# Kernel optimization log

Measured on AMD Instinct MI355X. Metric: run time of the kernel, lower is better.

## Reference

```python
import jax, jax.numpy as jnp
import numpy as np

D_MODEL = 512
N_STATE = 64
EMB_DIM = 512
LN_EPS = 1e-5


def setup_inputs() -> dict:
    key = jax.random.key(0)
    ks = jax.random.split(key, 12)
    B, L, d, N, e = 8, 2048, D_MODEL, N_STATE, EMB_DIM
    x = jax.random.normal(ks[0], (B, L, d), dtype=jnp.float32)
    emb = jax.random.normal(ks[1], (B, e), dtype=jnp.float32)
    # S4D kernel params
    A_real = -0.5 * jnp.ones((d, N), dtype=jnp.float32)
    A_imag = jnp.pi * jnp.broadcast_to(jnp.arange(N, dtype=jnp.float32)[None, :], (d, N))
    C = jax.random.normal(ks[2], (d, N, 2), dtype=jnp.float32) * 0.5
    dt_min, dt_max = 0.001, 0.1
    log_dt = jax.random.uniform(ks[3], (d,), dtype=jnp.float32) * (np.log(dt_max) - np.log(dt_min)) + np.log(dt_min)
    B_ssm = jnp.ones((d, N), dtype=jnp.float32)  # buffer, treated as constant
    # block params
    D_skip = jax.random.normal(ks[4], (d,), dtype=jnp.float32) * 0.01
    ln_gamma = jnp.ones((d,), dtype=jnp.float32)
    ln_beta = jnp.zeros((d,), dtype=jnp.float32)
    lim_out = 1.0 / np.sqrt(d)
    W_out = jax.random.uniform(ks[5], (2 * d, d), dtype=jnp.float32, minval=-lim_out, maxval=lim_out)
    b_out = jax.random.uniform(ks[6], (2 * d,), dtype=jnp.float32, minval=-lim_out, maxval=lim_out)
    lim_f = 1.0 / np.sqrt(e)
    W_film = jax.random.uniform(ks[7], (2 * d, e), dtype=jnp.float32, minval=-lim_f, maxval=lim_f)
    b_film = jax.random.uniform(ks[8], (2 * d,), dtype=jnp.float32, minval=-lim_f, maxval=lim_f)
    return dict(x=x, emb=emb, A_real=A_real, A_imag=A_imag, C=C, log_dt=log_dt,
                B_ssm=B_ssm, D_skip=D_skip, ln_gamma=ln_gamma, ln_beta=ln_beta,
                W_out=W_out, b_out=b_out, W_film=W_film, b_film=b_film)


def reference(x, emb, A_real, A_imag, C, log_dt, B_ssm, D_skip, ln_gamma, ln_beta,
              W_out, b_out, W_film, b_film):
    Bsz, L, d = x.shape
    residual = x
    # LayerNorm
    mu = jnp.mean(x, axis=-1, keepdims=True)
    var = jnp.mean((x - mu) ** 2, axis=-1, keepdims=True)
    xn = (x - mu) * jax.lax.rsqrt(var + LN_EPS) * ln_gamma + ln_beta
    # S4D kernel: K[d,l] = Re( sum_n (C*B)[d,n] * exp(dt*A)[d,n]**l ) * dt[d]
    dt = jnp.exp(log_dt)                                 # (d,)
    A = A_real + 1j * A_imag                             # (d,N)
    dtA = A * dt[:, None]                                # (d,N)
    Cc = (C[..., 0] + 1j * C[..., 1]) * B_ssm            # (d,N) complex
    l = jnp.arange(L, dtype=jnp.float32)
    powers = jnp.exp(dtA[:, :, None] * l)                # (d,N,L) complex, A_bar**l
    K = jnp.einsum('dn,dnl->dl', Cc, powers).real * dt[:, None]  # (d,L)
    # FFT convolution (circular over 2L -> linear)
    x_t = jnp.transpose(xn, (0, 2, 1))                   # (B,d,L)
    K_f = jnp.fft.rfft(K, n=2 * L)                       # (d,L+1)
    x_f = jnp.fft.rfft(x_t, n=2 * L)                     # (B,d,L+1)
    y = jnp.fft.irfft(K_f[None] * x_f, n=2 * L)[..., :L] # (B,d,L)
    y = y + x_t * D_skip[None, :, None]
    y = jnp.transpose(y, (0, 2, 1))                      # (B,L,d)
    # FiLM conditioning
    film = jax.nn.silu(emb) @ W_film.T + b_film          # (B,2d)
    scale, shift = jnp.split(film, 2, axis=-1)
    y = y * (1.0 + scale[:, None, :]) + shift[:, None, :]
    # out_proj: Linear(d,2d) + GLU
    proj = y @ W_out.T + b_out                           # (B,L,2d)
    a, g = jnp.split(proj, 2, axis=-1)
    y = a * jax.nn.sigmoid(g)
    return residual + y
```

## Files before the change

### kernel.cpp

```cpp
#include <hip/hip_runtime.h>
#include <math.h>

typedef __attribute__((ext_vector_type(8))) short bf8v;
typedef __attribute__((ext_vector_type(4))) float f4v;

union BF8 { bf8v v; unsigned short e[8]; };

__device__ __forceinline__ float bf2f(unsigned short u) {
  union { unsigned int i; float f; } c; c.i = ((unsigned int)u) << 16; return c.f;
}
__device__ __forceinline__ unsigned short f2bf(float f) {
  union { float f; unsigned int i; } c; c.f = f;
  return (unsigned short)((c.i + 0x7fffu + ((c.i >> 16) & 1u)) >> 16);
}
__device__ __forceinline__ void gld16(const unsigned short* g, unsigned short* l) {
  __builtin_amdgcn_global_load_lds(
      (const __attribute__((address_space(1))) unsigned int*)g,
      (__attribute__((address_space(3))) unsigned int*)l, 16, 0, 0);
}

__global__ __launch_bounds__(256) void prelude_kernel(
    const float* __restrict__ emb, const float* __restrict__ Wf,
    const float* __restrict__ bfm, float* __restrict__ film,
    const float* __restrict__ W, unsigned short* __restrict__ Wb,
    const float* __restrict__ A_real, const float* __restrict__ A_imag,
    const float* __restrict__ Cc, const float* __restrict__ log_dt,
    const float* __restrict__ B_ssm, const float* __restrict__ D_skip,
    unsigned short* __restrict__ Pre, unsigned short* __restrict__ Pim,
    unsigned short* __restrict__ Mre, unsigned short* __restrict__ Mim,
    unsigned short* __restrict__ Tt, float* __restrict__ W64r, float* __restrict__ W64i) {
  __shared__ float Ktl[64];
  const int blk = blockIdx.x;
  const int tid = threadIdx.x;
  if (blk < 2048) {
    const int gw = blk * 4 + (tid >> 6);
    const int lane = tid & 63;
    const int b = gw >> 10, j = gw & 1023;
    const float4* ep = (const float4*)(emb + (size_t)b * 512) + lane * 2;
    const float4* wp = (const float4*)(Wf + (size_t)j * 512) + lane * 2;
    float acc = 0.f;
    #pragma unroll
    for (int i = 0; i < 2; i++) {
      const float4 e = ep[i], w = wp[i];
      acc += (e.x / (1.f + __expf(-e.x))) * w.x;
      acc += (e.y / (1.f + __expf(-e.y))) * w.y;
      acc += (e.z / (1.f + __expf(-e.z))) * w.z;
      acc += (e.w / (1.f + __expf(-e.w))) * w.w;
    }
    #pragma unroll
    for (int off = 32; off >= 1; off >>= 1) acc += __shfl_xor(acc, off);
    if (lane == 0) film[(size_t)b * 1024 + j] = acc + bfm[j];
  } else if (blk < 2560) {
    const int i = (blk - 2048) * 256 + tid;
    const float4 v = ((const float4*)W)[i];
    uint2 pk;
    pk.x = (unsigned)f2bf(v.x) | ((unsigned)f2bf(v.y) << 16);
    pk.y = (unsigned)f2bf(v.z) | ((unsigned)f2bf(v.w) << 16);
    ((uint2*)Wb)[i] = pk;
  } else {
    const int d = blk - 2560;
    const float dt = __expf(log_dt[d]);
    const int wv = tid >> 6, n = tid & 63;
    {
      const int dn = d * 64 + n;
      const float ar = dt * A_real[dn], ai = dt * A_imag[dn];
      const float bs = B_ssm[dn] * dt;
      const float c0 = Cc[dn * 2] * bs, c1 = Cc[dn * 2 + 1] * bs;
      #pragma unroll
      for (int i = 0; i < 16; i++) {
        const float tau = (float)(wv * 16 + i);
        const float ex = __expf(ar * tau);
        float sn, cs; __sincosf(ai * tau, &sn, &cs);
        float r = ex * (c0 * cs - c1 * sn);
        #pragma unroll
        for (int off = 32; off >= 1; off >>= 1) r += __shfl_xor(r, off);
        if (n == 0) Ktl[wv * 16 + i] = (wv * 16 + i == 0) ? (r + D_skip[d]) : r;
      }
    }
    __syncthreads();
    for (int g = tid; g < 512; g += 256) {
      const int nn = g >> 3, s0 = (g & 7) * 8;
      const int dn = d * 64 + nn;
      const float ar = dt * A_real[dn], ai = dt * A_imag[dn];
      union { unsigned short s[8]; uint4 u; } pr, pi;
      #pragma unroll
      for (int j = 0; j < 8; j++) {
        const float k = (float)(63 - (s0 + j));
        const float ex = __expf(ar * k);
        float sn, cs; __sincosf(ai * k, &sn, &cs);
        pr.s[j] = f2bf(ex * cs); pi.s[j] = f2bf(ex * sn);
      }
      *(uint4*)(Pre + (size_t)d * 4096 + nn * 64 + s0) = pr.u;
      *(uint4*)(Pim + (size_t)d * 4096 + nn * 64 + s0) = pi.u;
    }
    for (int g = tid; g < 512; g += 256) {
      const int t = g >> 3, n0 = (g & 7) * 8;
      union { unsigned short s[8]; uint4 u; } mr, mi;
      #pragma unroll
      for (int j = 0; j < 8; j++) {
        const int dn = d * 64 + n0 + j;
        const float ar = dt * A_real[dn], ai = dt * A_imag[dn];
        const float bs = B_ssm[dn] * dt;
        const float c0 = Cc[dn * 2] * bs, c1 = Cc[dn * 2 + 1] * bs;
        const float k = (float)(t + 1);
        const float ex = __expf(ar * k);
        float sn, cs; __sincosf(ai * k, &sn, &cs);
        mr.s[j] = f2bf(ex * (c0 * cs - c1 * sn));
        mi.s[j] = f2bf(-ex * (c0 * sn + c1 * cs));
      }
      *(uint4*)(Mre + (size_t)d * 4096 + t * 64 + n0) = mr.u;
      *(uint4*)(Mim + (size_t)d * 4096 + t * 64 + n0) = mi.u;
    }
    for (int g = tid; g < 512; g += 256) {
      const int t = g >> 3, s0 = (g & 7) * 8;
      union { unsigned short s[8]; uint4 u; } tv;
      #pragma unroll
      for (int j = 0; j < 8; j++) {
        const int s = s0 + j;
        tv.s[j] = (s <= t) ? f2bf(Ktl[t - s]) : (unsigned short)0;
      }
      *(uint4*)(Tt + (size_t)d * 4096 + t * 64 + s0) = tv.u;
    }
    if (tid < 64) {
      const int dn = d * 64 + tid;
      const float ex = __expf(dt * A_real[dn] * 64.f);
      float sn, cs; __sincosf(dt * A_imag[dn] * 64.f, &sn, &cs);
      W64r[d * 64 + tid] = ex * cs;
      W64i[d * 64 + tid] = ex * sn;
    }
  }
}

__global__ __launch_bounds__(256) void lnt_kernel(const float* __restrict__ x,
    const float* __restrict__ gamma, const float* __restrict__ beta,
    unsigned short* __restrict__ xT) {
  __shared__ __align__(16) unsigned short t[16 * 520];
  const int r0 = blockIdx.x * 16;
  const int tid = threadIdx.x, wv = tid >> 6, lane = tid & 63;
  const float4* gp = (const float4*)gamma + lane * 2;
  const float4* bp = (const float4*)beta  + lane * 2;
  const float4 g0 = gp[0], g1 = gp[1], bb0 = bp[0], bb1 = bp[1];
  #pragma unroll
  for (int i = 0; i < 4; i++) {
    const int r = wv * 4 + i;
    const float4* xr = (const float4*)(x + (size_t)(r0 + r) * 512) + lane * 2;
    const float4 v0 = xr[0], v1 = xr[1];
    float s  = v0.x + v0.y + v0.z + v0.w + v1.x + v1.y + v1.z + v1.w;
    float sq = v0.x*v0.x + v0.y*v0.y + v0.z*v0.z + v0.w*v0.w
             + v1.x*v1.x + v1.y*v1.y + v1.z*v1.z + v1.w*v1.w;
    #pragma unroll
    for (int off = 32; off >= 1; off >>= 1) {
      s  += __shfl_xor(s, off);
      sq += __shfl_xor(sq, off);
    }
    const float mu   = s * (1.f / 512.f);
    const float var  = sq * (1.f / 512.f) - mu * mu;
    const float rstd = rsqrtf(var + 1e-5f);
    uint4 pk;
    pk.x = (unsigned)f2bf((v0.x - mu) * rstd * g0.x + bb0.x)
         | ((unsigned)f2bf((v0.y - mu) * rstd * g0.y + bb0.y) << 16);
    pk.y = (unsigned)f2bf((v0.z - mu) * rstd * g0.z + bb0.z)
         | ((unsigned)f2bf((v0.w - mu) * rstd * g0.w + bb0.w) << 16);
    pk.z = (unsigned)f2bf((v1.x - mu) * rstd * g1.x + bb1.x)
         | ((unsigned)f2bf((v1.y - mu) * rstd * g1.y + bb1.y) << 16);
    pk.w = (unsigned)f2bf((v1.z - mu) * rstd * g1.z + bb1.z)
         | ((unsigned)f2bf((v1.w - mu) * rstd * g1.w + bb1.w) << 16);
    *(uint4*)&t[r * 520 + lane * 8] = pk;
  }
  __syncthreads();
  const int p = tid;
  union { unsigned short s[8]; uint4 u; } a0, a1, b0, b1;
  #pragma unroll
  for (int r = 0; r < 8; r++) {
    const unsigned v = *(const unsigned*)&t[r * 520 + p * 2];
    a0.s[r] = (unsigned short)(v & 0xffffu);
    b0.s[r] = (unsigned short)(v >> 16);
  }
  #pragma unroll
  for (int r = 0; r < 8; r++) {
    const unsigned v = *(const unsigned*)&t[(r + 8) * 520 + p * 2];
    a1.s[r] = (unsigned short)(v & 0xffffu);
    b1.s[r] = (unsigned short)(v >> 16);
  }
  unsigned short* o0 = xT + (size_t)(2 * p) * 16384 + r0;
  *(uint4*)o0 = a0.u; *(uint4*)(o0 + 8) = a1.u;
  unsigned short* o1 = xT + (size_t)(2 * p + 1) * 16384 + r0;
  *(uint4*)o1 = b0.u; *(uint4*)(o1 + 8) = b1.u;
}

__global__ __launch_bounds__(256) void tr_kernel(const unsigned short* __restrict__ in,
    unsigned short* __restrict__ out, int R, int C) {
  __shared__ __align__(16) unsigned short t[64 * 72];
  const int c0 = blockIdx.x * 64, r0 = blockIdx.y * 64;
  const int tid = threadIdx.x;
  #pragma unroll
  for (int i = 0; i < 2; i++) {
    const int idx = tid + i * 256;
    const int r = idx >> 3, q = idx & 7;
    const uint4 v = *(const uint4*)(in + (size_t)(r0 + r) * C + c0 + q * 8);
    *(uint4*)&t[r * 72 + ((q ^ (r >> 3)) * 8)] = v;
  }
  __syncthreads();
  #pragma unroll
  for (int i = 0; i < 2; i++) {
    const int idx = tid + i * 256;
    const int c = idx >> 3, g = idx & 7;
    union { unsigned short s[8]; uint4 u; } pk;
    #pragma unroll
    for (int j = 0; j < 8; j++)
      pk.s[j] = t[(g * 8 + j) * 72 + (((c >> 3) ^ g) * 8) + (c & 7)];
    *(uint4*)(out + (size_t)(c0 + c) * R + r0 + g * 8) = pk.u;
  }
}

__global__ __launch_bounds__(256, 4) void ssm_kernel(
    const unsigned short* __restrict__ xT,
    const unsigned short* __restrict__ Pre, const unsigned short* __restrict__ Pim,
    const unsigned short* __restrict__ Mre, const unsigned short* __restrict__ Mim,
    const unsigned short* __restrict__ Tt,
    const float* __restrict__ W64r, const float* __restrict__ W64i,
    const float* __restrict__ film, unsigned short* __restrict__ y2) {
  __shared__ unsigned int Eb[64 * 66];
  __shared__ unsigned short Ibr[64 * 72], Ibi[64 * 72];

  const int bx = blockIdx.x;
  const int d = bx & 511, h = bx >> 9;
  const int tid = threadIdx.x;
  const int wv = tid >> 6, lane = tid & 63;
  const int n15 = lane & 15, quad = lane >> 4;
  const int j0 = wv * 16;
  const int jg0 = h * 64;
  const size_t dtab = (size_t)d * 4096;

  bf8v Xf[2];
  #pragma unroll
  for (int kq = 0; kq < 2; kq++)
    Xf[kq] = *(const bf8v*)(xT + (size_t)d * 16384 + (jg0 + j0 + n15) * 64 + kq * 32 + quad * 8);

  {
    f4v Er[4], Ei[4];
    #pragma unroll
    for (int a = 0; a < 4; a++) { Er[a] = (f4v){0,0,0,0}; Ei[a] = (f4v){0,0,0,0}; }
    #pragma unroll
    for (int mt = 0; mt < 4; mt++)
      #pragma unroll
      for (int kq = 0; kq < 2; kq++) {
        const bf8v pr = *(const bf8v*)(Pre + dtab + (mt * 16 + n15) * 64 + kq * 32 + quad * 8);
        const bf8v pi = *(const bf8v*)(Pim + dtab + (mt * 16 + n15) * 64 + kq * 32 + quad * 8);
        Er[mt] = __builtin_amdgcn_mfma_f32_16x16x32_bf16(pr, Xf[kq], Er[mt], 0, 0, 0);
        Ei[mt] = __builtin_amdgcn_mfma_f32_16x16x32_bf16(pi, Xf[kq], Ei[mt], 0, 0, 0);
      }
    #pragma unroll
    for (int mt = 0; mt < 4; mt++)
      #pragma unroll
      for (int i = 0; i < 4; i++) {
        const int row = mt * 16 + quad * 4 + i;
        Eb[row * 66 + j0 + n15] =
            (unsigned)f2bf(Er[mt][i]) | ((unsigned)f2bf(Ei[mt][i]) << 16);
      }
  }
  __syncthreads();

  {
    const int n = tid & 63, bp = tid >> 6;
    if (bp < 2) {
      const float wre = W64r[d * 64 + n], wim = W64i[d * 64 + n];
      unsigned int eb[32];
      #pragma unroll
      for (int c = 0; c < 32; c++) eb[c] = Eb[n * 66 + bp * 32 + c];
      float str = 0.f, sti = 0.f;
      #pragma unroll
      for (int c = 0; c < 32; c++) {
        const int j = bp * 32 + c;
        Ibr[j * 72 + n] = f2bf(str);
        Ibi[j * 72 + n] = f2bf(sti);
        const float er = bf2f((unsigned short)(eb[c] & 0xffffu));
        const float ei = bf2f((unsigned short)(eb[c] >> 16));
        const float nr = er + wre * str - wim * sti;
        const float ni = ei + wre * sti + wim * str;
        str = nr; sti = ni;
      }
    }
  }
  __syncthreads();

  f4v Y[4];
  #pragma unroll
  for (int a = 0; a < 4; a++) Y[a] = (f4v){0,0,0,0};

  #pragma unroll
  for (int mt = 0; mt < 4; mt++)
    #pragma unroll
    for (int kq = 0; kq < 2; kq++) {
      const bf8v tf = *(const bf8v*)(Tt + dtab + (mt * 16 + n15) * 64 + kq * 32 + quad * 8);
      Y[mt] = __builtin_amdgcn_mfma_f32_16x16x32_bf16(tf, Xf[kq], Y[mt], 0, 0, 0);
    }

  #pragma unroll
  for (int kq = 0; kq < 2; kq++) {
    const bf8v irf = *(const bf8v*)&Ibr[(j0 + n15) * 72 + kq * 32 + quad * 8];
    const bf8v iif = *(const bf8v*)&Ibi[(j0 + n15) * 72 + kq * 32 + quad * 8];
    #pragma unroll
    for (int mt = 0; mt < 4; mt++) {
      const bf8v mr = *(const bf8v*)(Mre + dtab + (mt * 16 + n15) * 64 + kq * 32 + quad * 8);
      const bf8v mi = *(const bf8v*)(Mim + dtab + (mt * 16 + n15) * 64 + kq * 32 + quad * 8);
      Y[mt] = __builtin_amdgcn_mfma_f32_16x16x32_bf16(mr, irf, Y[mt], 0, 0, 0);
      Y[mt] = __builtin_amdgcn_mfma_f32_16x16x32_bf16(mi, iif, Y[mt], 0, 0, 0);
    }
  }

  {
    const int jglob = jg0 + j0 + n15;
    const int b = jglob >> 5;
    const float scl = 1.f + film[b * 1024 + d];
    const float shf = film[b * 1024 + 512 + d];
    #pragma unroll
    for (int mt = 0; mt < 4; mt++) {
      union { unsigned short s[4]; uint2 u; } pk;
      #pragma unroll
      for (int i = 0; i < 4; i++)
        pk.s[i] = f2bf(fmaf(Y[mt][i], scl, shf));
      *(uint2*)(y2 + (size_t)d * 16384 + jglob * 64 + mt * 16 + quad * 4) = pk.u;
    }
  }
}

__global__ __launch_bounds__(256, 3) void gemm_kernel(
    const unsigned short* __restrict__ y2n, const unsigned short* __restrict__ Wb,
    const float* __restrict__ bo, const float* __restrict__ x,
    float* __restrict__ out) {
  __shared__ __align__(16) unsigned short Al[128 * 64];
  __shared__ __align__(16) unsigned short Bl[128 * 64];
  const int m0 = blockIdx.x * 128, ct = blockIdx.y;
  const int tid = threadIdx.x;
  const int wv = tid >> 6, lane = tid & 63;
  const int n15 = lane & 15, quad = lane >> 4;
  const int sr = lane >> 3;
  const int sk = ((lane & 7) ^ sr) * 8;

  f4v acc[2][8];
  #pragma unroll
  for (int mi = 0; mi < 2; mi++)
    #pragma unroll
    for (int t4 = 0; t4 < 8; t4++) acc[mi][t4] = (f4v){0.f, 0.f, 0.f, 0.f};

  for (int kk = 0; kk < 8; kk++) {
    #pragma unroll
    for (int c = 0; c < 4; c++) {
      const int row = wv * 32 + c * 8 + sr;
      gld16(y2n + (size_t)(m0 + row) * 512 + kk * 64 + sk, Al + wv * 2048 + c * 512);
      const int cg = (row < 64) ? (ct * 64 + row) : (512 + ct * 64 + (row - 64));
      gld16(Wb + (size_t)cg * 512 + kk * 64 + sk, Bl + wv * 2048 + c * 512);
    }
    __syncthreads();
    #pragma unroll
    for (int kq = 0; kq < 2; kq++) {
      const int r0 = wv * 32 + n15;
      const int r1 = r0 + 16;
      const bf8v a0 = *(const bf8v*)&Al[r0 * 64 + (((kq * 4 + quad) ^ (r0 & 7)) * 8)];
      const bf8v a1 = *(const bf8v*)&Al[r1 * 64 + (((kq * 4 + quad) ^ (r1 & 7)) * 8)];
      #pragma unroll
      for (int t4 = 0; t4 < 8; t4++) {
        const int rb = t4 * 16 + n15;
        const bf8v bb = *(const bf8v*)&Bl[rb * 64 + (((kq * 4 + quad) ^ (rb & 7)) * 8)];
        acc[0][t4] = __builtin_amdgcn_mfma_f32_16x16x32_bf16(a0, bb, acc[0][t4], 0, 0, 0);
        acc[1][t4] = __builtin_amdgcn_mfma_f32_16x16x32_bf16(a1, bb, acc[1][t4], 0, 0, 0);
      }
    }
    __syncthreads();
  }
  #pragma unroll
  for (int mi = 0; mi < 2; mi++) {
    const int mrow = m0 + wv * 32 + mi * 16 + quad * 4;
    #pragma unroll
    for (int t4 = 0; t4 < 4; t4++) {
      const int c = ct * 64 + t4 * 16 + n15;
      const float ba = bo[c], bg = bo[512 + c];
      #pragma unroll
      for (int i = 0; i < 4; i++) {
        const size_t off = (size_t)(mrow + i) * 512 + c;
        const float av = acc[mi][t4][i] + ba;
        const float gv = acc[mi][t4 + 4][i] + bg;
        out[off] = x[off] + av * (1.f / (1.f + __expf(-gv)));
      }
    }
  }
}

extern "C" void kernel_launch(void* const* d_in, const int* in_sizes, int n_in,
                              void* d_out, int out_size, void* d_ws, size_t ws_size,
                              hipStream_t stream) {
  const float* x      = (const float*)d_in[0];
  const float* emb    = (const float*)d_in[1];
  const float* A_real = (const float*)d_in[2];
  const float* A_imag = (const float*)d_in[3];
  const float* C      = (const float*)d_in[4];
  const float* log_dt = (const float*)d_in[5];
  const float* B_ssm  = (const float*)d_in[6];
  const float* D_skip = (const float*)d_in[7];
  const float* gamma  = (const float*)d_in[8];
  const float* beta   = (const float*)d_in[9];
  const float* W_out  = (const float*)d_in[10];
  const float* b_out  = (const float*)d_in[11];
  const float* W_film = (const float*)d_in[12];
  const float* b_film = (const float*)d_in[13];
  float* out = (float*)d_out;

  char* ws = (char*)d_ws;
  size_t o = 0;
  float*          film = (float*)(ws + o);          o += 32768;
  unsigned short* xT   = (unsigned short*)(ws + o); o += 16777216;
  unsigned short* Wb   = (unsigned short*)(ws + o); o += 1048576;
  unsigned short* Pre  = (unsigned short*)(ws + o); o += 4194304;
  unsigned short* Pim  = (unsigned short*)(ws + o); o += 4194304;
  unsigned short* Mre  = (unsigned short*)(ws + o); o += 4194304;
  unsigned short* Mim  = (unsigned short*)(ws + o); o += 4194304;
  unsigned short* Tt   = (unsigned short*)(ws + o); o += 4194304;
  float*          W64r = (float*)(ws + o);          o += 131072;
  float*          W64i = (float*)(ws + o);          o += 131072;
  unsigned short* y2   = (unsigned short*)(ws + o); o += 16777216;
  unsigned short* y2n  = (unsigned short*)(ws + o); o += 16777216;

  prelude_kernel<<<dim3(3072), dim3(256), 0, stream>>>(
      emb, W_film, b_film, film, W_out, Wb,
      A_real, A_imag, C, log_dt, B_ssm, D_skip,
      Pre, Pim, Mre, Mim, Tt, W64r, W64i);
  lnt_kernel<<<dim3(1024), dim3(256), 0, stream>>>(x, gamma, beta, xT);
  ssm_kernel<<<dim3(2048), dim3(256), 0, stream>>>(xT, Pre, Pim, Mre, Mim, Tt,
                                                   W64r, W64i, film, y2);
  tr_kernel<<<dim3(256, 8), dim3(256), 0, stream>>>(y2, y2n, 512, 16384);
  gemm_kernel<<<dim3(128, 8), dim3(256), 0, stream>>>(y2n, Wb, b_out, x, out);
}
```

Baseline: 196.4 us.

## Stage SSM chunk matrices in LDS and process two column tiles per wave

Each ssm_kernel block now copies the five per-channel 64x64 bf16 matrices (P, M, T) into shared memory once and covers 128 chunks instead of 64. Each wave handles two 16-column tiles, so every loaded matrix fragment feeds twice as many MFMAs. The grid is halved, and the global matrix reloads that were repeated across blocks and waves are removed. The inter-chunk scan now uses all four waves and writes its state back in place into the shared E buffer, replacing the separate Ibr/Ibi arrays. In exchange, the kernel needs about 77KB of dynamic shared memory and more registers, its launch bound drops to 2 blocks, and it loses occupancy. The transposed strided reads from Eb may also cause LDS bank conflicts.

```diff
diff --git a/kernel.cpp b/kernel.cpp
--- a/kernel.cpp
+++ b/kernel.cpp
@@ -213,104 +213,142 @@
   }
 }
 
-__global__ __launch_bounds__(256, 4) void ssm_kernel(
+__global__ __launch_bounds__(256, 2) void ssm_kernel(
     const unsigned short* __restrict__ xT,
     const unsigned short* __restrict__ Pre, const unsigned short* __restrict__ Pim,
     const unsigned short* __restrict__ Mre, const unsigned short* __restrict__ Mim,
     const unsigned short* __restrict__ Tt,
     const float* __restrict__ W64r, const float* __restrict__ W64i,
     const float* __restrict__ film, unsigned short* __restrict__ y2) {
-  __shared__ unsigned int Eb[64 * 66];
-  __shared__ unsigned short Ibr[64 * 72], Ibi[64 * 72];
+  extern __shared__ char smem[];
+  unsigned short* Pr = (unsigned short*)smem;
+  unsigned short* Pi = Pr + 64 * 68;
+  unsigned short* Mr = Pi + 64 * 68;
+  unsigned short* Mi = Mr + 64 * 68;
+  unsigned short* Tl = Mi + 64 * 68;
+  unsigned int*   Eb = (unsigned int*)(Tl + 64 * 68);
 
   const int bx = blockIdx.x;
   const int d = bx & 511, h = bx >> 9;
   const int tid = threadIdx.x;
   const int wv = tid >> 6, lane = tid & 63;
   const int n15 = lane & 15, quad = lane >> 4;
-  const int j0 = wv * 16;
-  const int jg0 = h * 64;
+  const int j0 = wv * 32;
+  const int jg0 = h * 128;
   const size_t dtab = (size_t)d * 4096;
 
-  bf8v Xf[2];
-  #pragma unroll
-  for (int kq = 0; kq < 2; kq++)
-    Xf[kq] = *(const bf8v*)(xT + (size_t)d * 16384 + (jg0 + j0 + n15) * 64 + kq * 32 + quad * 8);
-
   {
-    f4v Er[4], Ei[4];
-    #pragma unroll
-    for (int a = 0; a < 4; a++) { Er[a] = (f4v){0,0,0,0}; Ei[a] = (f4v){0,0,0,0}; }
+    const unsigned short* gt[5] = {Pre + dtab, Pim + dtab, Mre + dtab, Mim + dtab, Tt + dtab};
+    unsigned short* lt[5] = {Pr, Pi, Mr, Mi, Tl};
+    #pragma unroll
+    for (int i = 0; i < 10; i++) {
+      const int idx = tid + i * 256;
+      const int tb = idx >> 9, r = (idx >> 3) & 63, g = idx & 7;
+      const uint4 v = *(const uint4*)(gt[tb] + r * 64 + g * 8);
+      *(uint4*)&lt[tb][r * 68 + g * 8] = v;
+    }
+  }
+  bf8v Xf[2][2];
+  #pragma unroll
+  for (int ct = 0; ct < 2; ct++)
+    #pragma unroll
+    for (int kq = 0; kq < 2; kq++)
+      Xf[ct][kq] = *(const bf8v*)(xT + (size_t)d * 16384 +
+                                  (jg0 + j0 + ct * 16 + n15) * 64 + kq * 32 + quad * 8);
+  __syncthreads();
+
+  {
+    f4v Er[4][2], Ei[4][2];
+    #pragma unroll
+    for (int a = 0; a < 4; a++)
+      #pragma unroll
+      for (int b2 = 0; b2 < 2; b2++) { Er[a][b2] = (f4v){0,0,0,0}; Ei[a][b2] = (f4v){0,0,0,0}; }
     #pragma unroll
     for (int mt = 0; mt < 4; mt++)
       #pragma unroll
       for (int kq = 0; kq < 2; kq++) {
-        const bf8v pr = *(const bf8v*)(Pre + dtab + (mt * 16 + n15) * 64 + kq * 32 + quad * 8);
-        const bf8v pi = *(const bf8v*)(Pim + dtab + (mt * 16 + n15) * 64 + kq * 32 + quad * 8);
-        Er[mt] = __builtin_amdgcn_mfma_f32_16x16x32_bf16(pr, Xf[kq], Er[mt], 0, 0, 0);
-        Ei[mt] = __builtin_amdgcn_mfma_f32_16x16x32_bf16(pi, Xf[kq], Ei[mt], 0, 0, 0);
+        const bf8v pr = *(const bf8v*)&Pr[(mt * 16 + n15) * 68 + kq * 32 + quad * 8];
+        const bf8v pi = *(const bf8v*)&Pi[(mt * 16 + n15) * 68 + kq * 32 + quad * 8];
+        #pragma unroll
+        for (int ct = 0; ct < 2; ct++) {
+          Er[mt][ct] = __builtin_amdgcn_mfma_f32_16x16x32_bf16(pr, Xf[ct][kq], Er[mt][ct], 0, 0, 0);
+          Ei[mt][ct] = __builtin_amdgcn_mfma_f32_16x16x32_bf16(pi, Xf[ct][kq], Ei[mt][ct], 0, 0, 0);
+        }
       }
     #pragma unroll
     for (int mt = 0; mt < 4; mt++)
       #pragma unroll
-      for (int i = 0; i < 4; i++) {
-        const int row = mt * 16 + quad * 4 + i;
-        Eb[row * 66 + j0 + n15] =
-            (unsigned)f2bf(Er[mt][i]) | ((unsigned)f2bf(Ei[mt][i]) << 16);
-      }
+      for (int ct = 0; ct < 2; ct++)
+        #pragma unroll
+        for (int i = 0; i < 4; i++) {
+          const int row = mt * 16 + quad * 4 + i;
+          const int col = j0 + ct * 16 + n15;
+          Eb[row * 131 + col] =
+              (unsigned)f2bf(Er[mt][ct][i]) | ((unsigned)f2bf(Ei[mt][ct][i]) << 16);
+        }
   }
   __syncthreads();
 
   {
-    const int n = tid & 63, bp = tid >> 6;
-    if (bp < 2) {
-      const float wre = W64r[d * 64 + n], wim = W64i[d * 64 + n];
-      unsigned int eb[32];
-      #pragma unroll
-      for (int c = 0; c < 32; c++) eb[c] = Eb[n * 66 + bp * 32 + c];
-      float str = 0.f, sti = 0.f;
-      #pragma unroll
-      for (int c = 0; c < 32; c++) {
-        const int j = bp * 32 + c;
-        Ibr[j * 72 + n] = f2bf(str);
-        Ibi[j * 72 + n] = f2bf(sti);
-        const float er = bf2f((unsigned short)(eb[c] & 0xffffu));
-        const float ei = bf2f((unsigned short)(eb[c] >> 16));
-        const float nr = er + wre * str - wim * sti;
-        const float ni = ei + wre * sti + wim * str;
-        str = nr; sti = ni;
-      }
+    const int n = lane, bp = wv;
+    const float wre = W64r[d * 64 + n], wim = W64i[d * 64 + n];
+    unsigned int* row = &Eb[n * 131 + bp * 32];
+    float str = 0.f, sti = 0.f;
+    #pragma unroll
+    for (int c = 0; c < 32; c++) {
+      const unsigned u = row[c];
+      row[c] = (unsigned)f2bf(str) | ((unsigned)f2bf(sti) << 16);
+      const float er = bf2f((unsigned short)(u & 0xffffu));
+      const float ei = bf2f((unsigned short)(u >> 16));
+      const float nr = er + wre * str - wim * sti;
+      const float ni = ei + wre * sti + wim * str;
+      str = nr; sti = ni;
     }
   }
   __syncthreads();
 
-  f4v Y[4];
-  #pragma unroll
-  for (int a = 0; a < 4; a++) Y[a] = (f4v){0,0,0,0};
+  f4v Y[4][2];
+  #pragma unroll
+  for (int a = 0; a < 4; a++)
+    #pragma unroll
+    for (int b2 = 0; b2 < 2; b2++) Y[a][b2] = (f4v){0,0,0,0};
 
   #pragma unroll
   for (int mt = 0; mt < 4; mt++)
     #pragma unroll
     for (int kq = 0; kq < 2; kq++) {
-      const bf8v tf = *(const bf8v*)(Tt + dtab + (mt * 16 + n15) * 64 + kq * 32 + quad * 8);
-      Y[mt] = __builtin_amdgcn_mfma_f32_16x16x32_bf16(tf, Xf[kq], Y[mt], 0, 0, 0);
+      const bf8v tf = *(const bf8v*)&Tl[(mt * 16 + n15) * 68 + kq * 32 + quad * 8];
+      #pragma unroll
+      for (int ct = 0; ct < 2; ct++)
+        Y[mt][ct] = __builtin_amdgcn_mfma_f32_16x16x32_bf16(tf, Xf[ct][kq], Y[mt][ct], 0, 0, 0);
     }
 
   #pragma unroll
   for (int kq = 0; kq < 2; kq++) {
-    const bf8v irf = *(const bf8v*)&Ibr[(j0 + n15) * 72 + kq * 32 + quad * 8];
-    const bf8v iif = *(const bf8v*)&Ibi[(j0 + n15) * 72 + kq * 32 + quad * 8];
+    BF8 ir[2], ii[2];
+    #pragma unroll
+    for (int ct = 0; ct < 2; ct++)
+      #pragma unroll
+      for (int jj = 0; jj < 8; jj++) {
+        const unsigned u = Eb[(kq * 32 + quad * 8 + jj) * 131 + (j0 + ct * 16 + n15)];
+        ir[ct].e[jj] = (unsigned short)(u & 0xffffu);
+        ii[ct].e[jj] = (unsigned short)(u >> 16);
+      }
     #pragma unroll
     for (int mt = 0; mt < 4; mt++) {
-      const bf8v mr = *(const bf8v*)(Mre + dtab + (mt * 16 + n15) * 64 + kq * 32 + quad * 8);
-      const bf8v mi = *(const bf8v*)(Mim + dtab + (mt * 16 + n15) * 64 + kq * 32 + quad * 8);
-      Y[mt] = __builtin_amdgcn_mfma_f32_16x16x32_bf16(mr, irf, Y[mt], 0, 0, 0);
-      Y[mt] = __builtin_amdgcn_mfma_f32_16x16x32_bf16(mi, iif, Y[mt], 0, 0, 0);
-    }
-  }
-
-  {
-    const int jglob = jg0 + j0 + n15;
+      const bf8v mr = *(const bf8v*)&Mr[(mt * 16 + n15) * 68 + kq * 32 + quad * 8];
+      const bf8v mi = *(const bf8v*)&Mi[(mt * 16 + n15) * 68 + kq * 32 + quad * 8];
+      #pragma unroll
+      for (int ct = 0; ct < 2; ct++) {
+        Y[mt][ct] = __builtin_amdgcn_mfma_f32_16x16x32_bf16(mr, ir[ct].v, Y[mt][ct], 0, 0, 0);
+        Y[mt][ct] = __builtin_amdgcn_mfma_f32_16x16x32_bf16(mi, ii[ct].v, Y[mt][ct], 0, 0, 0);
+      }
+    }
+  }
+
+  #pragma unroll
+  for (int ct = 0; ct < 2; ct++) {
+    const int jglob = jg0 + j0 + ct * 16 + n15;
     const int b = jglob >> 5;
     const float scl = 1.f + film[b * 1024 + d];
     const float shf = film[b * 1024 + 512 + d];
@@ -319,7 +357,7 @@
       union { unsigned short s[4]; uint2 u; } pk;
       #pragma unroll
       for (int i = 0; i < 4; i++)
-        pk.s[i] = f2bf(fmaf(Y[mt][i], scl, shf));
+        pk.s[i] = f2bf(fmaf(Y[mt][ct][i], scl, shf));
       *(uint2*)(y2 + (size_t)d * 16384 + jglob * 64 + mt * 16 + quad * 4) = pk.u;
     }
   }
@@ -426,8 +464,8 @@
       A_real, A_imag, C, log_dt, B_ssm, D_skip,
       Pre, Pim, Mre, Mim, Tt, W64r, W64i);
   lnt_kernel<<<dim3(1024), dim3(256), 0, stream>>>(x, gamma, beta, xT);
-  ssm_kernel<<<dim3(2048), dim3(256), 0, stream>>>(xT, Pre, Pim, Mre, Mim, Tt,
-                                                   W64r, W64i, film, y2);
+  ssm_kernel<<<dim3(1024), dim3(256), 77056, stream>>>(xT, Pre, Pim, Mre, Mim, Tt,
+                                                       W64r, W64i, film, y2);
   tr_kernel<<<dim3(256, 8), dim3(256), 0, stream>>>(y2, y2n, 512, 16384);
   gemm_kernel<<<dim3(128, 8), dim3(256), 0, stream>>>(y2n, Wb, b_out, x, out);
 }
```

After: 193.3 us. No clear change (-1.6%).
